# Kernel optimization log

Hardware: AMD Instinct MI355X
Metric: run time of the kernel (lower is better)

Reference implementation:

```python
import jax, jax.numpy as jnp
import numpy as np

# 4x4 Walsh-Hadamard matrix in natural (Hadamard/Kronecker) order: H4 = H2 (x) H2
_H4 = jnp.array([[1, 1, 1, 1],
                 [1, -1, 1, -1],
                 [1, 1, -1, -1],
                 [1, -1, -1, 1]], dtype=jnp.float32)

T = 16          # number of 2D WHT coefficients (4x4 block)
BLK = 4         # spatial block size


def _iwht_stream(trans, weight):
    """trans: (16, B, nH, nW, C); weight: (16, C, K) -> out: (B, 4*nH, 4*nW, K).

    Per-coefficient channel mixing in the transform domain, then inverse 2D
    Walsh-Hadamard transform (separable, scale 1/16) back to spatial domain.
    """
    _, B, nH, nW, C = trans.shape
    K = weight.shape[2]
    # transform-domain channel mixing: (t,b,h,w,c) x (t,c,k) -> (t,b,h,w,k)
    mixed = jnp.einsum('tbhwc,tck->tbhwk', trans, weight)
    # split coefficient index t = 4*u + v (row/col frequency)
    mixed = mixed.reshape(BLK, BLK, B, nH, nW, K)
    # inverse separable WHT: out[b,nh,i,nw,j,k] = (1/16) sum_{u,v} H4[i,u] H4[j,v] mixed[u,v,...]
    out = jnp.einsum('iu,jv,uvbhwk->bhiwjk', _H4, _H4, mixed) * (1.0 / 16.0)
    return out.reshape(B, nH * BLK, nW * BLK, K)


def setup_inputs() -> dict:
    key = jax.random.key(0)
    k1, k2, k3, k4 = jax.random.split(key, 4)
    B, nH, nW, C = 16, 28, 28, 64
    out_channels = 128
    K1 = out_channels // 2
    K2 = out_channels // 2 + out_channels % 2
    transIm1 = jax.random.normal(k1, (T, B, nH, nW, C), dtype=jnp.float32)
    transIm2 = jax.random.normal(k2, (T, B, nH, nW, C), dtype=jnp.float32)
    weight1 = jax.random.normal(k3, (T, C, K1), dtype=jnp.float32) * 0.02
    weight2 = jax.random.normal(k4, (T, C, K2), dtype=jnp.float32) * 0.02
    bias1 = jnp.zeros((1, 1, 1, K1), dtype=jnp.float32)
    bias2 = jnp.zeros((1, 1, 1, K2), dtype=jnp.float32)
    return {"transIm1": transIm1, "transIm2": transIm2,
            "weight1": weight1, "weight2": weight2,
            "bias1": bias1, "bias2": bias2}


def reference(transIm1, transIm2, weight1, weight2, bias1, bias2):
    out1 = _iwht_stream(transIm1, weight1) + bias1
    out2 = _iwht_stream(transIm2, weight2) + bias2
    return (out1, out2)
```

## Files before the change

kernel.cpp:

```cpp
#include <hip/hip_runtime.h>
#include <hip/hip_bf16.h>

typedef float f32x4 __attribute__((ext_vector_type(4)));
typedef short s16x8 __attribute__((ext_vector_type(8)));

#define NPIX       12544
#define TPLANE     802816
#define OUT_STRIDE 12845056

__device__ __forceinline__ unsigned short f2bf(float x) {
    union { float f; unsigned u; } un; un.f = x;
    unsigned r = un.u + 0x7FFFu + ((un.u >> 16) & 1u);
    return (unsigned short)(r >> 16);
}

__device__ __forceinline__ short bfs(float x) {
    __hip_bfloat16 h = __float2bfloat16(x);
    return *reinterpret_cast<short*>(&h);
}

__global__ __launch_bounds__(256) void repack_weights(
        const float* __restrict__ w1, const float* __restrict__ w2,
        unsigned short* __restrict__ wf) {
    int gid = blockIdx.x * 256 + threadIdx.x;
    int k = gid & 63;
    int c = (gid >> 6) & 63;
    int t = (gid >> 12) & 15;
    int s = (gid >> 16) & 1;
    const float* __restrict__ w = s ? w2 : w1;
    float val = w[gid & 65535] * 0.0625f;
    int e = c & 7, lhi = (c >> 3) & 3, ks = c >> 5;
    int l  = lhi * 16 + (k & 15);
    int nt = k >> 4;
    int dst = ((((s * 16 + t) * 2 + ks) * 4 + nt) * 64 + l) * 8 + e;
    wf[dst] = f2bf(val);
}

__global__ __launch_bounds__(256, 4) void iwht_main(
        const float* __restrict__ trans1, const float* __restrict__ trans2,
        const unsigned short* __restrict__ wf,
        const float* __restrict__ bias1, const float* __restrict__ bias2,
        float* __restrict__ out) {
    const int tid = threadIdx.x;
    const int bid = blockIdx.x;
    const int s   = blockIdx.y;

    const int wid  = tid >> 6;
    const int lane = tid & 63;
    const int lrow = lane & 15;
    const int lhi  = lane >> 4;

    const float* __restrict__ trans = s ? trans2 : trans1;
    const float* __restrict__ bias  = s ? bias2  : bias1;

    const f32x4* __restrict__ abase =
        (const f32x4*)(trans + ((size_t)(bid * 16 + lrow)) * 64 + lhi * 8);

    const s16x8* __restrict__ wb =
        (const s16x8*)wf + (size_t)s * 8192 + wid * 64 + lane;

    f32x4 o[4][4];
    #pragma unroll
    for (int i = 0; i < 4; ++i)
        #pragma unroll
        for (int j = 0; j < 4; ++j)
            o[i][j] = (f32x4){0.f, 0.f, 0.f, 0.f};

    #pragma unroll 1
    for (int u = 0; u < 4; ++u) {
        f32x4 st[4][4];
        #pragma unroll
        for (int v = 0; v < 4; ++v) {
            const int t = u * 4 + v;
            const f32x4* ap = abase + (size_t)t * (TPLANE / 4);
            st[v][0] = ap[0];
            st[v][1] = ap[1];
            st[v][2] = ap[8];
            st[v][3] = ap[9];
        }
        f32x4 g0 = {0.f,0.f,0.f,0.f}, g1 = {0.f,0.f,0.f,0.f};
        f32x4 g2 = {0.f,0.f,0.f,0.f}, g3 = {0.f,0.f,0.f,0.f};
        #pragma unroll
        for (int v = 0; v < 4; ++v) {
            const int t = u * 4 + v;
            s16x8 a0, a1;
            #pragma unroll
            for (int e = 0; e < 4; ++e) {
                a0[e]     = bfs(st[v][0][e]);
                a0[e + 4] = bfs(st[v][1][e]);
                a1[e]     = bfs(st[v][2][e]);
                a1[e + 4] = bfs(st[v][3][e]);
            }
            s16x8 b0 = wb[t * 512];
            s16x8 b1 = wb[t * 512 + 256];
            f32x4 acc = {0.f, 0.f, 0.f, 0.f};
            acc = __builtin_amdgcn_mfma_f32_16x16x32_bf16(a0, b0, acc, 0, 0, 0);
            acc = __builtin_amdgcn_mfma_f32_16x16x32_bf16(a1, b1, acc, 0, 0, 0);
            g0 += acc;
            if (v == 0) { g1 += acc; g2 += acc; g3 += acc; }
            if (v == 1) { g1 -= acc; g2 += acc; g3 -= acc; }
            if (v == 2) { g1 += acc; g2 -= acc; g3 -= acc; }
            if (v == 3) { g1 -= acc; g2 -= acc; g3 += acc; }
        }
        const float s1 = (u & 1) ? -1.f : 1.f;
        const float s2 = (u & 2) ? -1.f : 1.f;
        const float s3 = s1 * s2;
        #pragma unroll
        for (int j = 0; j < 4; ++j) {
            f32x4 gj = (j == 0) ? g0 : ((j == 1) ? g1 : ((j == 2) ? g2 : g3));
            o[0][j] += gj;
            o[1][j] += s1 * gj;
            o[2][j] += s2 * gj;
            o[3][j] += s3 * gj;
        }
    }

    const int k  = wid * 16 + lrow;
    const float bk = bias[k];
    const int bimg = bid / 49;
    const int hw0  = (bid % 49) * 16;
    float* __restrict__ outp = out + (s ? (size_t)OUT_STRIDE : 0);

    size_t rbase[4];
    #pragma unroll
    for (int r = 0; r < 4; ++r) {
        int hw = hw0 + lhi * 4 + r;
        int h = hw / 28, w = hw % 28;
        rbase[r] = ((size_t)(bimg * 112 + h * 4) * 112 + (w * 4)) * 64 + k;
    }
    #pragma unroll
    for (int i = 0; i < 4; ++i)
        #pragma unroll
        for (int j = 0; j < 4; ++j) {
            #pragma unroll
            for (int r = 0; r < 4; ++r)
                outp[rbase[r] + (size_t)((i * 112 + j) * 64)] = o[i][j][r] + bk;
        }
}

extern "C" void kernel_launch(void* const* d_in, const int* in_sizes, int n_in,
                              void* d_out, int out_size, void* d_ws, size_t ws_size,
                              hipStream_t stream) {
    const float* t1 = (const float*)d_in[0];
    const float* t2 = (const float*)d_in[1];
    const float* w1 = (const float*)d_in[2];
    const float* w2 = (const float*)d_in[3];
    const float* b1 = (const float*)d_in[4];
    const float* b2 = (const float*)d_in[5];
    unsigned short* wfrag = (unsigned short*)d_ws;
    float* out = (float*)d_out;

    repack_weights<<<dim3(512), dim3(256), 0, stream>>>(w1, w2, wfrag);
    iwht_main<<<dim3(784, 2), dim3(256), 0, stream>>>(t1, t2, wfrag, b1, b2, out);
}
```

Before: 243.5 us.

## Stage inputs via LDS direct loads and coalesce output stores through LDS

Converts the kernel to a persistent grid of 512 blocks that loop over tiles from both streams. Activation tiles are loaded asynchronously into a 64KB LDS buffer with global_load_lds, and weight fragments are double-buffered in registers. Results are written to swizzled LDS and then stored as coalesced 16-byte rows instead of scattered scalar stores. The inverse WHT combine is rewritten as a butterfly. The larger LDS use cuts occupancy to 2 blocks per CU and adds barriers per tile.

```diff
diff --git a/kernel.cpp b/kernel.cpp
--- a/kernel.cpp
+++ b/kernel.cpp
@@ -5,8 +5,9 @@
 typedef short s16x8 __attribute__((ext_vector_type(8)));
 
 #define NPIX       12544
-#define TPLANE     802816
 #define OUT_STRIDE 12845056
+#define NTILES     1568
+#define GRIDX      512
 
 __device__ __forceinline__ unsigned short f2bf(float x) {
     union { float f; unsigned u; } un; un.f = x;
@@ -17,6 +18,12 @@
 __device__ __forceinline__ short bfs(float x) {
     __hip_bfloat16 h = __float2bfloat16(x);
     return *reinterpret_cast<short*>(&h);
+}
+
+__device__ __forceinline__ void gload_lds16(const void* g, void* l) {
+    __builtin_amdgcn_global_load_lds(
+        (const __attribute__((address_space(1))) unsigned int*)g,
+        (__attribute__((address_space(3))) unsigned int*)l, 16, 0, 0);
 }
 
 __global__ __launch_bounds__(256) void repack_weights(
@@ -36,106 +43,147 @@
     wf[dst] = f2bf(val);
 }
 
-__global__ __launch_bounds__(256, 4) void iwht_main(
+__global__ __launch_bounds__(256, 2) void iwht_main(
         const float* __restrict__ trans1, const float* __restrict__ trans2,
         const unsigned short* __restrict__ wf,
         const float* __restrict__ bias1, const float* __restrict__ bias2,
         float* __restrict__ out) {
-    const int tid = threadIdx.x;
-    const int bid = blockIdx.x;
-    const int s   = blockIdx.y;
-
+    __shared__ __align__(16) unsigned char lds[65536];
+
+    const int tid  = threadIdx.x;
     const int wid  = tid >> 6;
     const int lane = tid & 63;
     const int lrow = lane & 15;
     const int lhi  = lane >> 4;
 
-    const float* __restrict__ trans = s ? trans2 : trans1;
-    const float* __restrict__ bias  = s ? bias2  : bias1;
-
-    const f32x4* __restrict__ abase =
-        (const f32x4*)(trans + ((size_t)(bid * 16 + lrow)) * 64 + lhi * 8);
-
-    const s16x8* __restrict__ wb =
-        (const s16x8*)wf + (size_t)s * 8192 + wid * 64 + lane;
-
-    f32x4 o[4][4];
-    #pragma unroll
-    for (int i = 0; i < 4; ++i)
-        #pragma unroll
-        for (int j = 0; j < 4; ++j)
-            o[i][j] = (f32x4){0.f, 0.f, 0.f, 0.f};
-
-    #pragma unroll 1
-    for (int u = 0; u < 4; ++u) {
-        f32x4 st[4][4];
+    const s16x8* __restrict__ wbb = (const s16x8*)wf;
+
+    for (int tau = blockIdx.x; tau < NTILES; tau += GRIDX) {
+        const int s   = (tau >= 784) ? 1 : 0;
+        const int bid = tau - s * 784;
+        const float* __restrict__ trans = s ? trans2 : trans1;
+        const int p0 = bid * 16;
+
+        {
+            const int ks = wid >> 1, j = wid & 1;
+            const float* g0 = trans + (size_t)(p0 + lrow) * 64
+                                    + (ks * 8 + lhi * 2 + j) * 4;
+            #pragma unroll
+            for (int t = 0; t < 16; ++t)
+                gload_lds16(g0 + (size_t)t * (NPIX * 64),
+                            lds + t * 4096 + wid * 1024);
+        }
+
+        const s16x8* __restrict__ wb = wbb + (size_t)s * 8192 + wid * 64 + lane;
+        s16x8 bA[8], bB[8];
         #pragma unroll
         for (int v = 0; v < 4; ++v) {
-            const int t = u * 4 + v;
-            const f32x4* ap = abase + (size_t)t * (TPLANE / 4);
-            st[v][0] = ap[0];
-            st[v][1] = ap[1];
-            st[v][2] = ap[8];
-            st[v][3] = ap[9];
-        }
-        f32x4 g0 = {0.f,0.f,0.f,0.f}, g1 = {0.f,0.f,0.f,0.f};
-        f32x4 g2 = {0.f,0.f,0.f,0.f}, g3 = {0.f,0.f,0.f,0.f};
-        #pragma unroll
-        for (int v = 0; v < 4; ++v) {
-            const int t = u * 4 + v;
-            s16x8 a0, a1;
-            #pragma unroll
-            for (int e = 0; e < 4; ++e) {
-                a0[e]     = bfs(st[v][0][e]);
-                a0[e + 4] = bfs(st[v][1][e]);
-                a1[e]     = bfs(st[v][2][e]);
-                a1[e + 4] = bfs(st[v][3][e]);
+            bA[v]     = wb[(size_t)(v * 8 + 0) * 64];
+            bA[4 + v] = wb[(size_t)(v * 8 + 4) * 64];
+        }
+
+        f32x4 o[4][4];
+        #pragma unroll
+        for (int i = 0; i < 4; ++i)
+            #pragma unroll
+            for (int j = 0; j < 4; ++j)
+                o[i][j] = (f32x4){0.f, 0.f, 0.f, 0.f};
+
+        __syncthreads();
+
+        #pragma unroll 1
+        for (int uu = 0; uu < 4; uu += 2) {
+            #pragma unroll
+            for (int v = 0; v < 4; ++v) {
+                int t = (uu + 1) * 4 + v;
+                bB[v]     = wb[(size_t)(t * 8 + 0) * 64];
+                bB[4 + v] = wb[(size_t)(t * 8 + 4) * 64];
             }
-            s16x8 b0 = wb[t * 512];
-            s16x8 b1 = wb[t * 512 + 256];
-            f32x4 acc = {0.f, 0.f, 0.f, 0.f};
-            acc = __builtin_amdgcn_mfma_f32_16x16x32_bf16(a0, b0, acc, 0, 0, 0);
-            acc = __builtin_amdgcn_mfma_f32_16x16x32_bf16(a1, b1, acc, 0, 0, 0);
-            g0 += acc;
-            if (v == 0) { g1 += acc; g2 += acc; g3 += acc; }
-            if (v == 1) { g1 -= acc; g2 += acc; g3 -= acc; }
-            if (v == 2) { g1 += acc; g2 -= acc; g3 -= acc; }
-            if (v == 3) { g1 -= acc; g2 -= acc; g3 += acc; }
-        }
-        const float s1 = (u & 1) ? -1.f : 1.f;
-        const float s2 = (u & 2) ? -1.f : 1.f;
-        const float s3 = s1 * s2;
-        #pragma unroll
-        for (int j = 0; j < 4; ++j) {
-            f32x4 gj = (j == 0) ? g0 : ((j == 1) ? g1 : ((j == 2) ? g2 : g3));
-            o[0][j] += gj;
-            o[1][j] += s1 * gj;
-            o[2][j] += s2 * gj;
-            o[3][j] += s3 * gj;
-        }
+            #pragma unroll
+            for (int half = 0; half < 2; ++half) {
+                const int u = uu + half;
+                f32x4 acc[4];
+                #pragma unroll
+                for (int v = 0; v < 4; ++v) {
+                    const int t = u * 4 + v;
+                    const unsigned char* ab = lds + t * 4096 + lane * 16;
+                    f32x4 q0 = *(const f32x4*)(ab);
+                    f32x4 q1 = *(const f32x4*)(ab + 1024);
+                    f32x4 q2 = *(const f32x4*)(ab + 2048);
+                    f32x4 q3 = *(const f32x4*)(ab + 3072);
+                    s16x8 a0, a1;
+                    #pragma unroll
+                    for (int e = 0; e < 4; ++e) {
+                        a0[e] = bfs(q0[e]); a0[4 + e] = bfs(q1[e]);
+                        a1[e] = bfs(q2[e]); a1[4 + e] = bfs(q3[e]);
+                    }
+                    f32x4 tacc = {0.f, 0.f, 0.f, 0.f};
+                    if (half == 0) {
+                        tacc = __builtin_amdgcn_mfma_f32_16x16x32_bf16(a0, bA[v],     tacc, 0, 0, 0);
+                        tacc = __builtin_amdgcn_mfma_f32_16x16x32_bf16(a1, bA[4 + v], tacc, 0, 0, 0);
+                    } else {
+                        tacc = __builtin_amdgcn_mfma_f32_16x16x32_bf16(a0, bB[v],     tacc, 0, 0, 0);
+                        tacc = __builtin_amdgcn_mfma_f32_16x16x32_bf16(a1, bB[4 + v], tacc, 0, 0, 0);
+                    }
+                    acc[v] = tacc;
+                }
+                if (half == 0 && uu + 2 < 4) {
+                    #pragma unroll
+                    for (int v = 0; v < 4; ++v) {
+                        int t = (uu + 2) * 4 + v;
+                        bA[v]     = wb[(size_t)(t * 8 + 0) * 64];
+                        bA[4 + v] = wb[(size_t)(t * 8 + 4) * 64];
+                    }
+                }
+                f32x4 e0 = acc[0] + acc[1], e1 = acc[0] - acc[1];
+                f32x4 e2 = acc[2] + acc[3], e3 = acc[2] - acc[3];
+                f32x4 g0 = e0 + e2, g1 = e1 + e3, g2 = e0 - e2, g3 = e1 - e3;
+                const float s1 = (u & 1) ? -1.f : 1.f;
+                const float s2 = (u & 2) ? -1.f : 1.f;
+                const float s3 = s1 * s2;
+                #pragma unroll
+                for (int j = 0; j < 4; ++j) {
+                    f32x4 gj = (j == 0) ? g0 : ((j == 1) ? g1 : ((j == 2) ? g2 : g3));
+                    o[0][j] += gj;
+                    o[1][j] += s1 * gj;
+                    o[2][j] += s2 * gj;
+                    o[3][j] += s3 * gj;
+                }
+            }
+        }
+
+        const float* __restrict__ bias = s ? bias2 : bias1;
+        const int k = wid * 16 + lrow;
+        const float bk = bias[k];
+        __syncthreads();
+        #pragma unroll
+        for (int i = 0; i < 4; ++i)
+            #pragma unroll
+            for (int j = 0; j < 4; ++j)
+                #pragma unroll
+                for (int r = 0; r < 4; ++r) {
+                    int p = lhi * 4 + r;
+                    int w = k ^ (4 * (p & 7)) ^ (16 * (j & 1));
+                    *(float*)(lds + p * 4096 + i * 1024 + j * 256 + w * 4) = o[i][j][r] + bk;
+                }
+        __syncthreads();
+        const int bimg = bid / 49;
+        const int hw0  = (bid % 49) * 16;
+        float* __restrict__ outp = out + (s ? (size_t)OUT_STRIDE : 0);
+        #pragma unroll
+        for (int n = 0; n < 16; ++n) {
+            int idx = wid * 16 + n;
+            int p = idx >> 2, i = idx & 3;
+            int hw = hw0 + p;
+            int h = hw / 28, w = hw % 28;
+            size_t rowbase = ((size_t)(bimg * 112 + h * 4 + i) * 112 + w * 4) * 64;
+            int g = (lane & 15) ^ (p & 7) ^ (4 * ((lane >> 4) & 1));
+            f32x4 val = *(const f32x4*)(lds + p * 4096 + i * 1024
+                                        + (lane >> 4) * 256 + g * 16);
+            *(f32x4*)(outp + rowbase + lane * 4) = val;
+        }
+        __syncthreads();
     }
-
-    const int k  = wid * 16 + lrow;
-    const float bk = bias[k];
-    const int bimg = bid / 49;
-    const int hw0  = (bid % 49) * 16;
-    float* __restrict__ outp = out + (s ? (size_t)OUT_STRIDE : 0);
-
-    size_t rbase[4];
-    #pragma unroll
-    for (int r = 0; r < 4; ++r) {
-        int hw = hw0 + lhi * 4 + r;
-        int h = hw / 28, w = hw % 28;
-        rbase[r] = ((size_t)(bimg * 112 + h * 4) * 112 + (w * 4)) * 64 + k;
-    }
-    #pragma unroll
-    for (int i = 0; i < 4; ++i)
-        #pragma unroll
-        for (int j = 0; j < 4; ++j) {
-            #pragma unroll
-            for (int r = 0; r < 4; ++r)
-                outp[rbase[r] + (size_t)((i * 112 + j) * 64)] = o[i][j][r] + bk;
-        }
 }
 
 extern "C" void kernel_launch(void* const* d_in, const int* in_sizes, int n_in,
@@ -151,5 +199,5 @@
     float* out = (float*)d_out;
 
     repack_weights<<<dim3(512), dim3(256), 0, stream>>>(w1, w2, wfrag);
-    iwht_main<<<dim3(784, 2), dim3(256), 0, stream>>>(t1, t2, wfrag, b1, b2, out);
-}
+    iwht_main<<<dim3(GRIDX), dim3(256), 0, stream>>>(t1, t2, wfrag, b1, b2, out);
+}
```

Measured after the change: 202.7 us. 1.2x faster.
